# Kernel tuning notes

Hardware: AMD Instinct MI355X
Metric: run time of the kernel (lower is better)

The kernel has to match this reference:

```python
import jax, jax.numpy as jnp
import numpy as np

N_HEAD = 16
N_EMBD = 1024
SPARSE_BLOCK = 64  # band width: keys j with i-64 <= j <= i are visible
B, T = 2, 2048


def setup_inputs() -> dict:
    key = jax.random.key(0)
    ks = jax.random.split(key, 5)
    C = N_EMBD
    scale = 0.02
    return {
        "x": jax.random.normal(ks[0], (B, T, C), dtype=jnp.float32),
        "Wqkv": jax.random.normal(ks[1], (C, 3 * C), dtype=jnp.float32) * scale,
        "bqkv": jnp.zeros((3 * C,), dtype=jnp.float32),
        "Wproj": jax.random.normal(ks[2], (C, C), dtype=jnp.float32) * scale,
        "bproj": jnp.zeros((C,), dtype=jnp.float32),
    }


def reference(x, Wqkv, bqkv, Wproj, bproj):
    Bz, Tz, C = x.shape
    H, D = N_HEAD, C // N_HEAD
    qkv = x @ Wqkv + bqkv                       # [B,T,3C]
    q, k, v = jnp.split(qkv, 3, axis=-1)

    def heads(t):  # [B,T,C] -> [B,H,T,D]
        return t.reshape(Bz, Tz, H, D).transpose(0, 2, 1, 3)
    q, k, v = heads(q), heads(k), heads(v)

    scale = 1.0 / jnp.sqrt(jnp.float32(D))
    att = jnp.einsum("bhtd,bhsd->bhts", q, k) * scale  # [B,H,T,T]

    # causal + local band mask: key j visible to query i iff i-64 <= j <= i
    i = jnp.arange(Tz)[:, None]
    j = jnp.arange(Tz)[None, :]
    mask = (j <= i) & (j >= i - SPARSE_BLOCK)           # [T,T] bool
    att = jnp.where(mask[None, None], att, -jnp.inf)
    att = jax.nn.softmax(att, axis=-1)

    y = jnp.einsum("bhts,bhsd->bhtd", att, v)           # [B,H,T,D]
    y = y.transpose(0, 2, 1, 3).reshape(Bz, Tz, C)
    return y @ Wproj + bproj
```

## Files before the change

### kernel.cpp

```cpp
#include <hip/hip_runtime.h>
#include <hip/hip_bf16.h>
#include <math.h>

#define N_HEAD 16
#define N_EMBD 1024
#define HEADD  64
#define BANDW  64
#define BB     2
#define TT     2048

typedef __attribute__((ext_vector_type(8))) short bf16x8;
typedef __attribute__((ext_vector_type(4))) float f32x4;

__device__ __forceinline__ ushort f2b(float f) {
    __hip_bfloat16 h = __float2bfloat16(f);
    union { __hip_bfloat16 h; ushort u; } cv; cv.h = h; return cv.u;
}
__device__ __forceinline__ float b2f(ushort u) { return __uint_as_float(((unsigned)u) << 16); }

#define GLOAD16(gp, lp) \
    __builtin_amdgcn_global_load_lds((const __attribute__((address_space(1))) void*)(gp), \
                                     (__attribute__((address_space(3))) void*)(lp), 16, 0, 0)

__global__ __launch_bounds__(256) void k_prep(
    const float* __restrict__ x, ushort* __restrict__ xb,
    const float* __restrict__ Wqkv, ushort* __restrict__ wqkvT,
    const float* __restrict__ Wproj, ushort* __restrict__ wprojT)
{
    __shared__ float tile[32][33];
    int bid = blockIdx.x;
    int t = threadIdx.x;
    if (bid < 4096) {
        int i = bid * 256 + t;
        float4 v = reinterpret_cast<const float4*>(x)[i];
        ushort4 o;
        o.x = f2b(v.x); o.y = f2b(v.y); o.z = f2b(v.z); o.w = f2b(v.w);
        reinterpret_cast<ushort4*>(xb)[i] = o;
        return;
    }
    const float* in; ushort* out; int R, C, bx, by;
    if (bid < 4096 + 3072) {
        int b2 = bid - 4096;
        in = Wqkv; out = wqkvT; R = 1024; C = 3072;
        bx = b2 % 96; by = b2 / 96;
    } else {
        int b3 = bid - 7168;
        in = Wproj; out = wprojT; R = 1024; C = 1024;
        bx = b3 & 31; by = b3 >> 5;
    }
    int tx = t & 31, ty = t >> 5;
    int c0 = bx * 32, r0 = by * 32;
    for (int rr = ty; rr < 32; rr += 8)
        tile[rr][tx] = in[(size_t)(r0 + rr) * C + (c0 + tx)];
    __syncthreads();
    for (int cc = ty; cc < 32; cc += 8)
        out[(size_t)(c0 + cc) * R + (r0 + tx)] = f2b(tile[tx][cc]);
}

template <bool OUT_BF16>
__global__ __launch_bounds__(512, 4) void k_gemm1(
    const ushort* __restrict__ A, const ushort* __restrict__ BT,
    const float* __restrict__ bias, void* __restrict__ Cout,
    int M, int N, int K)
{
    __shared__ __align__(16) char lds[81920];
    const int K2 = K * 2;
    int t = threadIdx.x, lane = t & 63, w = t >> 6;
    int wm = w >> 2, wn = w & 3;
    int lr = lane & 15, kg = lane >> 4;

    int nbx = N / 192;
    int cpx = gridDim.x >> 3;
    int wg = blockIdx.x;
    int wgid = (wg & 7) * cpx + (wg >> 3);
    int bx = wgid % nbx, by = wgid / nbx;
    int row0 = by * 128, col0 = bx * 192;

    size_t sA0, sA1, sB0, sB1, sB2;
    {
        int o = w * 2048 + lane * 16;
        int r = o >> 7, c = ((o >> 4) - r) & 7;
        sA0 = (size_t)r * K2 + c * 16;
        o += 1024; r = o >> 7; c = ((o >> 4) - r) & 7;
        sA1 = (size_t)r * K2 + c * 16;
        int ob = w * 3072 + lane * 16;
        int rb = ob >> 7, cb = ((ob >> 4) - rb) & 7;
        sB0 = (size_t)rb * K2 + cb * 16;
        ob += 1024; rb = ob >> 7; cb = ((ob >> 4) - rb) & 7;
        sB1 = (size_t)rb * K2 + cb * 16;
        ob += 1024; rb = ob >> 7; cb = ((ob >> 4) - rb) & 7;
        sB2 = (size_t)rb * K2 + cb * 16;
    }
    const char* gA = (const char*)A  + (size_t)row0 * K2;
    const char* gB = (const char*)BT + (size_t)col0 * K2;

    int offA[4][2], offB[3][2];
#pragma unroll
    for (int m = 0; m < 4; ++m) {
        int rr = wm * 64 + m * 16 + lr;
#pragma unroll
        for (int ks = 0; ks < 2; ++ks)
            offA[m][ks] = rr * 128 + (((ks * 4 + kg) + rr) & 7) * 16;
    }
#pragma unroll
    for (int n = 0; n < 3; ++n) {
        int rr = wn * 48 + n * 16 + lr;
#pragma unroll
        for (int ks = 0; ks < 2; ++ks)
            offB[n][ks] = rr * 128 + (((ks * 4 + kg) + rr) & 7) * 16;
    }

    f32x4 acc[4][3];
#pragma unroll
    for (int i = 0; i < 4; ++i)
#pragma unroll
        for (int j = 0; j < 3; ++j) { f32x4 z = {0.f, 0.f, 0.f, 0.f}; acc[i][j] = z; }

#define STAGE1(BUF, TI) do { \
        char* _db = lds + (BUF) * 40960; \
        const char* _ga = gA + (size_t)(TI) * 128; \
        const char* _gb = gB + (size_t)(TI) * 128; \
        GLOAD16(_ga + sA0, _db + w * 2048); \
        GLOAD16(_ga + sA1, _db + w * 2048 + 1024); \
        GLOAD16(_gb + sB0, _db + 16384 + w * 3072); \
        GLOAD16(_gb + sB1, _db + 16384 + w * 3072 + 1024); \
        GLOAD16(_gb + sB2, _db + 16384 + w * 3072 + 2048); \
    } while (0)

    STAGE1(0, 0);
    __syncthreads();

    int nt = K >> 6;
#pragma unroll 2
    for (int tt = 0; tt < nt; ++tt) {
        int cur = tt & 1;
        if (tt + 1 < nt) STAGE1(cur ^ 1, tt + 1);
        const char* bufb = lds + cur * 40960;
#pragma unroll
        for (int ks = 0; ks < 2; ++ks) {
            bf16x8 af[4], bfr[3];
#pragma unroll
            for (int m = 0; m < 4; ++m)
                af[m] = *(const bf16x8*)(bufb + offA[m][ks]);
#pragma unroll
            for (int n = 0; n < 3; ++n)
                bfr[n] = *(const bf16x8*)(bufb + 16384 + offB[n][ks]);
#pragma unroll
            for (int m = 0; m < 4; ++m)
#pragma unroll
                for (int n = 0; n < 3; ++n)
                    acc[m][n] = __builtin_amdgcn_mfma_f32_16x16x32_bf16(
                        af[m], bfr[n], acc[m][n], 0, 0, 0);
        }
        __syncthreads();
    }
#undef STAGE1

#pragma unroll
    for (int m = 0; m < 4; ++m) {
        int growb = row0 + wm * 64 + m * 16 + kg * 4;
#pragma unroll
        for (int n = 0; n < 3; ++n) {
            int gcol = col0 + wn * 48 + n * 16 + lr;
            float bv = bias ? bias[gcol] : 0.f;
#pragma unroll
            for (int e = 0; e < 4; ++e) {
                float val = acc[m][n][e] + bv;
                if (OUT_BF16)
                    ((ushort*)Cout)[(size_t)(growb + e) * N + gcol] = f2b(val);
                else
                    ((float*)Cout)[(size_t)(growb + e) * N + gcol] = val;
            }
        }
    }
}

template <bool OUT_BF16>
__global__ __launch_bounds__(512, 4) void k_gemm2(
    const ushort* __restrict__ A, const ushort* __restrict__ BT,
    const float* __restrict__ bias, void* __restrict__ Cout,
    int M, int N, int K)
{
    __shared__ __align__(16) char lds[65536];
    const int K2 = K * 2;
    int t = threadIdx.x, lane = t & 63, w = t >> 6;
    int wm = w >> 2, wn = w & 3;
    int lr = lane & 15, kg = lane >> 4;

    int nbx = N >> 7;
    int cpx = gridDim.x >> 3;
    int wg = blockIdx.x;
    int wgid = (wg & 7) * cpx + (wg >> 3);
    int bx = wgid % nbx, by = wgid / nbx;
    int row0 = by * 128, col0 = bx * 128;

    size_t sA0, sA1;
    {
        int o = w * 2048 + lane * 16;
        int r = o >> 7, c = ((o >> 4) - r) & 7;
        sA0 = (size_t)r * K2 + c * 16;
        o += 1024; r = o >> 7; c = ((o >> 4) - r) & 7;
        sA1 = (size_t)r * K2 + c * 16;
    }
    const char* gA = (const char*)A  + (size_t)row0 * K2;
    const char* gB = (const char*)BT + (size_t)col0 * K2;

    int offA[4][2], offB[2][2];
#pragma unroll
    for (int m = 0; m < 4; ++m) {
        int rr = wm * 64 + m * 16 + lr;
#pragma unroll
        for (int ks = 0; ks < 2; ++ks)
            offA[m][ks] = rr * 128 + (((ks * 4 + kg) + rr) & 7) * 16;
    }
#pragma unroll
    for (int n = 0; n < 2; ++n) {
        int rr = wn * 32 + n * 16 + lr;
#pragma unroll
        for (int ks = 0; ks < 2; ++ks)
            offB[n][ks] = rr * 128 + (((ks * 4 + kg) + rr) & 7) * 16;
    }

    f32x4 acc[4][2];
#pragma unroll
    for (int i = 0; i < 4; ++i)
#pragma unroll
        for (int j = 0; j < 2; ++j) { f32x4 z = {0.f, 0.f, 0.f, 0.f}; acc[i][j] = z; }

#define STAGE2(BUF, TI) do { \
        char* _db = lds + (BUF) * 32768; \
        const char* _ga = gA + (size_t)(TI) * 128; \
        const char* _gb = gB + (size_t)(TI) * 128; \
        GLOAD16(_ga + sA0, _db + w * 2048); \
        GLOAD16(_ga + sA1, _db + w * 2048 + 1024); \
        GLOAD16(_gb + sA0, _db + 16384 + w * 2048); \
        GLOAD16(_gb + sA1, _db + 16384 + w * 2048 + 1024); \
    } while (0)

    STAGE2(0, 0);
    __syncthreads();

    int nt = K >> 6;
#pragma unroll 2
    for (int tt = 0; tt < nt; ++tt) {
        int cur = tt & 1;
        if (tt + 1 < nt) STAGE2(cur ^ 1, tt + 1);
        const char* bufb = lds + cur * 32768;
#pragma unroll
        for (int ks = 0; ks < 2; ++ks) {
            bf16x8 af[4], bfr[2];
#pragma unroll
            for (int m = 0; m < 4; ++m)
                af[m] = *(const bf16x8*)(bufb + offA[m][ks]);
#pragma unroll
            for (int n = 0; n < 2; ++n)
                bfr[n] = *(const bf16x8*)(bufb + 16384 + offB[n][ks]);
#pragma unroll
            for (int m = 0; m < 4; ++m)
#pragma unroll
                for (int n = 0; n < 2; ++n)
                    acc[m][n] = __builtin_amdgcn_mfma_f32_16x16x32_bf16(
                        af[m], bfr[n], acc[m][n], 0, 0, 0);
        }
        __syncthreads();
    }
#undef STAGE2

#pragma unroll
    for (int m = 0; m < 4; ++m) {
        int growb = row0 + wm * 64 + m * 16 + kg * 4;
#pragma unroll
        for (int n = 0; n < 2; ++n) {
            int gcol = col0 + wn * 32 + n * 16 + lr;
            float bv = bias ? bias[gcol] : 0.f;
#pragma unroll
            for (int e = 0; e < 4; ++e) {
                float val = acc[m][n][e] + bv;
                if (OUT_BF16)
                    ((ushort*)Cout)[(size_t)(growb + e) * N + gcol] = f2b(val);
                else
                    ((float*)Cout)[(size_t)(growb + e) * N + gcol] = val;
            }
        }
    }
}

__global__ __launch_bounds__(256) void k_attn(const ushort* __restrict__ qkv,
                                              ushort* __restrict__ y) {
    __shared__ __align__(16) ushort Ks[128 * 64];
    __shared__ ushort Vt[64][136];
    __shared__ ushort Ps[64][136];

    const int R3 = 3 * N_EMBD;
    int bid = blockIdx.x;
    int l  = (bid & 7) * 128 + (bid >> 3);
    int qt = l & 31;
    int h  = (l >> 5) & (N_HEAD - 1);
    int b  = l >> 9;
    int i0 = qt * 64;
    int j0 = i0 - BANDW;
    int hc = h * HEADD;

    int t    = threadIdx.x;
    int lane = t & 63;
    int wq   = t >> 6;
    int lr   = lane & 15;
    int kg   = lane >> 4;

    const ushort* kbase_g = qkv + (size_t)b * TT * R3 + N_EMBD + hc;
#pragma unroll
    for (int rnd = 0; rnd < 4; ++rnd) {
        int o = wq * 4096 + rnd * 1024 + lane * 16;
        int row  = o >> 7;
        int cblk = (((o >> 4) & 7) - row) & 7;
        int j = j0 + row; if (j < 0) j = 0;
        GLOAD16((const char*)(kbase_g + (size_t)j * R3) + cblk * 16,
                (char*)Ks + wq * 4096 + rnd * 1024);
    }

    {
        int row  = t >> 1;
        int part = t & 1;
        int j = j0 + row;
        if (j >= 0) {
            const ushort* vrow = qkv + (size_t)(b * TT + j) * R3 + 2 * N_EMBD + hc + part * 32;
#pragma unroll
            for (int c = 0; c < 4; ++c) {
                uint4 vv = reinterpret_cast<const uint4*>(vrow)[c];
                const ushort* pv = (const ushort*)&vv;
                int dbase = part * 32 + c * 8;
#pragma unroll
                for (int e = 0; e < 8; ++e)
                    Vt[dbase + e][row] = pv[e];
            }
        } else {
#pragma unroll
            for (int c = 0; c < 4; ++c) {
                int dbase = part * 32 + c * 8;
#pragma unroll
                for (int e = 0; e < 8; ++e)
                    Vt[dbase + e][row] = 0;
            }
        }
    }

    const ushort* qbase = qkv + (size_t)(b * TT + i0 + wq * 16 + lr) * R3 + hc;
    bf16x8 aq0 = *reinterpret_cast<const bf16x8*>(qbase + kg * 8);
    bf16x8 aq1 = *reinterpret_cast<const bf16x8*>(qbase + 32 + kg * 8);

    __syncthreads();

    f32x4 s[8];
#pragma unroll
    for (int nt = 0; nt < 8; ++nt) { f32x4 z = {0.f, 0.f, 0.f, 0.f}; s[nt] = z; }
#pragma unroll
    for (int nt = 0; nt < 8; ++nt) {
        int row = nt * 16 + lr;
        const char* kr = (const char*)Ks + row * 128;
        bf16x8 kb0 = *(const bf16x8*)(kr + (((kg)     + row) & 7) * 16);
        bf16x8 kb1 = *(const bf16x8*)(kr + (((4 + kg) + row) & 7) * 16);
        s[nt] = __builtin_amdgcn_mfma_f32_16x16x32_bf16(aq0, kb0, s[nt], 0, 0, 0);
        s[nt] = __builtin_amdgcn_mfma_f32_16x16x32_bf16(aq1, kb1, s[nt], 0, 0, 0);
    }

    float mx[4] = {-INFINITY, -INFINITY, -INFINITY, -INFINITY};
#pragma unroll
    for (int nt = 0; nt < 8; ++nt) {
        int kc = nt * 16 + lr;
#pragma unroll
        for (int e = 0; e < 4; ++e) {
            int qr = wq * 16 + kg * 4 + e;
            bool valid = (kc >= qr) && (kc <= qr + BANDW) && (j0 + kc >= 0);
            float v = s[nt][e] * 0.125f;
            s[nt][e] = valid ? v : -INFINITY;
            mx[e] = fmaxf(mx[e], s[nt][e]);
        }
    }
#pragma unroll
    for (int e = 0; e < 4; ++e) {
#pragma unroll
        for (int m = 1; m <= 8; m <<= 1)
            mx[e] = fmaxf(mx[e], __shfl_xor(mx[e], m, 64));
    }
    float sm[4] = {0.f, 0.f, 0.f, 0.f};
#pragma unroll
    for (int nt = 0; nt < 8; ++nt) {
        int kc = nt * 16 + lr;
#pragma unroll
        for (int e = 0; e < 4; ++e) {
            float p = __expf(s[nt][e] - mx[e]);
            sm[e] += p;
            Ps[wq * 16 + kg * 4 + e][kc] = f2b(p);
        }
    }
#pragma unroll
    for (int e = 0; e < 4; ++e) {
#pragma unroll
        for (int m = 1; m <= 8; m <<= 1)
            sm[e] += __shfl_xor(sm[e], m, 64);
    }

    f32x4 o[4];
#pragma unroll
    for (int vt = 0; vt < 4; ++vt) { f32x4 z = {0.f, 0.f, 0.f, 0.f}; o[vt] = z; }
#pragma unroll
    for (int ks = 0; ks < 4; ++ks) {
        bf16x8 pa = *reinterpret_cast<const bf16x8*>(&Ps[wq * 16 + lr][ks * 32 + kg * 8]);
#pragma unroll
        for (int vt = 0; vt < 4; ++vt) {
            bf16x8 vb = *reinterpret_cast<const bf16x8*>(&Vt[vt * 16 + lr][ks * 32 + kg * 8]);
            o[vt] = __builtin_amdgcn_mfma_f32_16x16x32_bf16(pa, vb, o[vt], 0, 0, 0);
        }
    }

    float inv[4];
#pragma unroll
    for (int e = 0; e < 4; ++e) inv[e] = 1.f / sm[e];

#pragma unroll
    for (int vt = 0; vt < 4; ++vt) {
#pragma unroll
        for (int e = 0; e < 4; ++e) {
            int qr = wq * 16 + kg * 4 + e;
            y[(size_t)(b * TT + i0 + qr) * N_EMBD + hc + vt * 16 + lr] =
                f2b(o[vt][e] * inv[e]);
        }
    }
}

extern "C" void kernel_launch(void* const* d_in, const int* in_sizes, int n_in,
                              void* d_out, int out_size, void* d_ws, size_t ws_size,
                              hipStream_t stream) {
    const float* x     = (const float*)d_in[0];
    const float* Wqkv  = (const float*)d_in[1];
    const float* bqkv  = (const float*)d_in[2];
    const float* Wproj = (const float*)d_in[3];
    const float* bproj = (const float*)d_in[4];
    float* out = (float*)d_out;

    const int M  = BB * TT;
    const int C  = N_EMBD;
    const int N1 = 3 * C;

    char* ws = (char*)d_ws;
    ushort* xb     = (ushort*)ws; ws += (size_t)M  * C * 2;
    ushort* wqkvT  = (ushort*)ws; ws += (size_t)N1 * C * 2;
    ushort* wprojT = (ushort*)ws; ws += (size_t)C  * C * 2;
    ushort* qkvb   = (ushort*)ws; ws += (size_t)M  * N1 * 2;
    ushort* yb     = (ushort*)ws; ws += (size_t)M  * C * 2;

    k_prep<<<8192, 256, 0, stream>>>(x, xb, Wqkv, wqkvT, Wproj, wprojT);
    {
        int nwg = (M / 128) * (N1 / 192);
        k_gemm1<true><<<nwg, 512, 0, stream>>>(xb, wqkvT, bqkv, (void*)qkvb, M, N1, C);
    }
    k_attn<<<BB * N_HEAD * (TT / 64), 256, 0, stream>>>(qkvb, yb);
    {
        int nwg = (M / 128) * (C / 128);
        k_gemm2<false><<<nwg, 512, 0, stream>>>(yb, wprojT, bproj, (void*)out, M, C, C);
    }
}
```

Before: 69.72 us.

## Triple-buffer GEMM LDS pipeline with explicit vmcnt waits and MFMA priority

```diff
diff --git a/kernel.cpp b/kernel.cpp
--- a/kernel.cpp
+++ b/kernel.cpp
@@ -58,12 +58,12 @@
 }
 
 template <bool OUT_BF16>
-__global__ __launch_bounds__(512, 4) void k_gemm1(
+__global__ __launch_bounds__(512, 2) void k_gemm1(
     const ushort* __restrict__ A, const ushort* __restrict__ BT,
     const float* __restrict__ bias, void* __restrict__ Cout,
     int M, int N, int K)
 {
-    __shared__ __align__(16) char lds[81920];
+    __shared__ __align__(16) char lds[3 * 40960];
     const int K2 = K * 2;
     int t = threadIdx.x, lane = t & 63, w = t >> 6;
     int wm = w >> 2, wn = w & 3;
@@ -116,8 +116,8 @@
 #pragma unroll
         for (int j = 0; j < 3; ++j) { f32x4 z = {0.f, 0.f, 0.f, 0.f}; acc[i][j] = z; }
 
-#define STAGE1(BUF, TI) do { \
-        char* _db = lds + (BUF) * 40960; \
+#define STAGE1(DB, TI) do { \
+        char* _db = (DB); \
         const char* _ga = gA + (size_t)(TI) * 128; \
         const char* _gb = gB + (size_t)(TI) * 128; \
         GLOAD16(_ga + sA0, _db + w * 2048); \
@@ -127,15 +127,22 @@
         GLOAD16(_gb + sB2, _db + 16384 + w * 3072 + 2048); \
     } while (0)
 
-    STAGE1(0, 0);
-    __syncthreads();
-
     int nt = K >> 6;
-#pragma unroll 2
+    STAGE1(lds, 0);
+    if (nt > 1) STAGE1(lds + 40960, 1);
+
+#pragma unroll 3
     for (int tt = 0; tt < nt; ++tt) {
-        int cur = tt & 1;
-        if (tt + 1 < nt) STAGE1(cur ^ 1, tt + 1);
-        const char* bufb = lds + cur * 40960;
+        const char* bufb = lds + (size_t)(tt % 3) * 40960;
+        if (tt + 2 < nt) {
+            STAGE1(lds + (size_t)((tt + 2) % 3) * 40960, tt + 2);
+            asm volatile("s_waitcnt vmcnt(10)" ::: "memory");
+        } else if (tt + 1 < nt) {
+            asm volatile("s_waitcnt vmcnt(5)" ::: "memory");
+        } else {
+            asm volatile("s_waitcnt vmcnt(0)" ::: "memory");
+        }
+        __builtin_amdgcn_s_barrier();
 #pragma unroll
         for (int ks = 0; ks < 2; ++ks) {
             bf16x8 af[4], bfr[3];
@@ -145,14 +152,17 @@
 #pragma unroll
             for (int n = 0; n < 3; ++n)
                 bfr[n] = *(const bf16x8*)(bufb + 16384 + offB[n][ks]);
+            __builtin_amdgcn_s_setprio(1);
 #pragma unroll
             for (int m = 0; m < 4; ++m)
 #pragma unroll
                 for (int n = 0; n < 3; ++n)
                     acc[m][n] = __builtin_amdgcn_mfma_f32_16x16x32_bf16(
                         af[m], bfr[n], acc[m][n], 0, 0, 0);
-        }
-        __syncthreads();
+            __builtin_amdgcn_s_setprio(0);
+        }
+        asm volatile("s_waitcnt lgkmcnt(0)" ::: "memory");
+        __builtin_amdgcn_s_barrier();
     }
 #undef STAGE1
 
@@ -176,12 +186,12 @@
 }
 
 template <bool OUT_BF16>
-__global__ __launch_bounds__(512, 4) void k_gemm2(
+__global__ __launch_bounds__(512, 2) void k_gemm2(
     const ushort* __restrict__ A, const ushort* __restrict__ BT,
     const float* __restrict__ bias, void* __restrict__ Cout,
     int M, int N, int K)
 {
-    __shared__ __align__(16) char lds[65536];
+    __shared__ __align__(16) char lds[3 * 32768];
     const int K2 = K * 2;
     int t = threadIdx.x, lane = t & 63, w = t >> 6;
     int wm = w >> 2, wn = w & 3;
@@ -227,8 +237,8 @@
 #pragma unroll
         for (int j = 0; j < 2; ++j) { f32x4 z = {0.f, 0.f, 0.f, 0.f}; acc[i][j] = z; }
 
-#define STAGE2(BUF, TI) do { \
-        char* _db = lds + (BUF) * 32768; \
+#define STAGE2(DB, TI) do { \
+        char* _db = (DB); \
         const char* _ga = gA + (size_t)(TI) * 128; \
         const char* _gb = gB + (size_t)(TI) * 128; \
         GLOAD16(_ga + sA0, _db + w * 2048); \
@@ -237,15 +247,22 @@
         GLOAD16(_gb + sA1, _db + 16384 + w * 2048 + 1024); \
     } while (0)
 
-    STAGE2(0, 0);
-    __syncthreads();
-
     int nt = K >> 6;
-#pragma unroll 2
+    STAGE2(lds, 0);
+    if (nt > 1) STAGE2(lds + 32768, 1);
+
+#pragma unroll 3
     for (int tt = 0; tt < nt; ++tt) {
-        int cur = tt & 1;
-        if (tt + 1 < nt) STAGE2(cur ^ 1, tt + 1);
-        const char* bufb = lds + cur * 32768;
+        const char* bufb = lds + (size_t)(tt % 3) * 32768;
+        if (tt + 2 < nt) {
+            STAGE2(lds + (size_t)((tt + 2) % 3) * 32768, tt + 2);
+            asm volatile("s_waitcnt vmcnt(8)" ::: "memory");
+        } else if (tt + 1 < nt) {
+            asm volatile("s_waitcnt vmcnt(4)" ::: "memory");
+        } else {
+            asm volatile("s_waitcnt vmcnt(0)" ::: "memory");
+        }
+        __builtin_amdgcn_s_barrier();
 #pragma unroll
         for (int ks = 0; ks < 2; ++ks) {
             bf16x8 af[4], bfr[2];
@@ -255,14 +272,17 @@
 #pragma unroll
             for (int n = 0; n < 2; ++n)
                 bfr[n] = *(const bf16x8*)(bufb + 16384 + offB[n][ks]);
+            __builtin_amdgcn_s_setprio(1);
 #pragma unroll
             for (int m = 0; m < 4; ++m)
 #pragma unroll
                 for (int n = 0; n < 2; ++n)
                     acc[m][n] = __builtin_amdgcn_mfma_f32_16x16x32_bf16(
                         af[m], bfr[n], acc[m][n], 0, 0, 0);
-        }
-        __syncthreads();
+            __builtin_amdgcn_s_setprio(0);
+        }
+        asm volatile("s_waitcnt lgkmcnt(0)" ::: "memory");
+        __builtin_amdgcn_s_barrier();
     }
 #undef STAGE2
 
```

Result: slower. 80.42 us (+15.3%).
